# Kernel optimization log

Hardware: AMD Instinct MI355X
Metric: run time of the kernel (lower is better)

Reference implementation:

```python
import jax, jax.numpy as jnp
import numpy as np

WS = 10      # window_size
HID = 32     # hidden_dim
B, T = 1024, 4096


def setup_inputs() -> dict:
    key = jax.random.key(0)
    k = jax.random.split(key, 7)
    returns = jax.random.normal(k[0], (B, T), dtype=jnp.float32) * 0.01
    W1 = jax.random.normal(k[1], (WS, HID), dtype=jnp.float32) * (1.0 / np.sqrt(WS))
    b1 = jnp.zeros((HID,), dtype=jnp.float32)
    W2 = jax.random.normal(k[2], (HID, HID), dtype=jnp.float32) * (1.0 / np.sqrt(HID))
    b2 = jnp.zeros((HID,), dtype=jnp.float32)
    W3 = jax.random.normal(k[3], (HID, 1), dtype=jnp.float32) * (1.0 / np.sqrt(HID))
    b3 = jnp.zeros((1,), dtype=jnp.float32)
    return {"returns": returns, "W1": W1, "b1": b1, "W2": W2, "b2": b2, "W3": W3, "b3": b3}


def reference(returns, W1, b1, W2, b2, W3, b3):
    ws = W1.shape[0]
    Bb, Tt = returns.shape
    # Unfold all sliding windows at once: windows[b, i, :] = returns[b, i:i+ws]
    # (window ending just before timestep t = i + ws)
    idx = jnp.arange(Tt - ws)[:, None] + jnp.arange(ws)[None, :]  # [T-ws, ws]
    windows = returns[:, idx]                                     # [B, T-ws, ws]
    h = jax.nn.relu(windows @ W1 + b1)                            # [B, T-ws, HID]
    h = jax.nn.relu(h @ W2 + b2)                                  # [B, T-ws, HID]
    out = 0.5 * jax.nn.sigmoid((h @ W3 + b3).squeeze(-1))         # [B, T-ws]
    # H_local[:, t] = out[:, t-ws] for t >= ws; first ws columns copy column ws
    head = jnp.broadcast_to(out[:, :1], (Bb, ws))                 # [B, ws]
    return jnp.concatenate([head, out], axis=1)                   # [B, T]
```

## Files before the change

### kernel.cpp

```cpp
#include <hip/hip_runtime.h>
#include <math.h>

typedef _Float16 f16x8  __attribute__((ext_vector_type(8)));
typedef float    f32x16 __attribute__((ext_vector_type(16)));
typedef float    f32x4  __attribute__((ext_vector_type(4)));
typedef __fp16   h2a    __attribute__((ext_vector_type(2)));
typedef unsigned u32x4  __attribute__((ext_vector_type(4)));

#define WS    10
#define HID   32
#define BDIM  256
#define NWAVE 4
#define GN    32
#define TILE  1024
#define NGRP  (TILE / GN)

__device__ inline unsigned pack2u(float a, float b) {
    h2a t = __builtin_amdgcn_cvt_pkrtz(a, b);
    return __builtin_bit_cast(unsigned, t);
}

__global__ __launch_bounds__(BDIM, 2)
void hurst_mlp_mfma32v2(const float* __restrict__ returns,
                        const float* __restrict__ W1, const float* __restrict__ b1,
                        const float* __restrict__ W2, const float* __restrict__ b2,
                        const float* __restrict__ W3, const float* __restrict__ b3,
                        float* __restrict__ out, int T)
{
    __shared__ float sret[TILE + WS];
    __shared__ __align__(16) _Float16 Xh[TILE][16];

    const int tid  = threadIdx.x;
    const int wid  = tid >> 6;
    const int lane = tid & 63;
    const int n    = lane & 31;
    const int hi   = lane >> 5;
    const int permidx = (lane ^ 32) << 2;

    f32x16 b1v, b2v, w3v;
    #pragma unroll
    for (int i = 0; i < 4; ++i) {
        const f32x4 v1 = ((const f32x4*)b1)[2 * i + hi];
        const f32x4 v2 = ((const f32x4*)b2)[2 * i + hi];
        const f32x4 v3 = ((const f32x4*)W3)[2 * i + hi];
        #pragma unroll
        for (int o = 0; o < 4; ++o) {
            b1v[4 * i + o] = v1[o];
            b2v[4 * i + o] = v2[o];
            w3v[4 * i + o] = v3[o];
        }
    }
    const float b3s = b3[0];

    f16x8 a1, a2lo, a2hi;
    #pragma unroll
    for (int jj = 0; jj < 8; ++jj) {
        const int k  = 8 * hi + jj;
        a1[jj] = (k < WS) ? (_Float16)W1[k * HID + n] : (_Float16)0.0f;
        const int kf = (k & 3) | ((k & 4) << 1) | ((k & 8) >> 1);
        a2lo[jj] = (_Float16)W2[kf * HID + n];
        a2hi[jj] = (_Float16)W2[(16 + kf) * HID + n];
    }

    const int    b    = blockIdx.y;
    const int    t0   = blockIdx.x * TILE;
    const int    base = (t0 >= WS) ? (t0 - WS) : 0;
    const size_t row  = (size_t)b * (size_t)T;

    for (int i = tid; i < TILE + WS; i += BDIM) {
        int g = base + i;
        sret[i] = (g < T) ? returns[row + g] : 0.0f;
    }
    __syncthreads();

    #pragma unroll
    for (int i = 0; i < TILE / BDIM; ++i) {
        const int m   = tid + i * BDIM;
        const int t   = t0 + m;
        const int off = (t >= WS) ? (t - WS - base) : 0;
        u32x4 lo, hi4;
        lo[0]  = pack2u(sret[off + 0], sret[off + 1]);
        lo[1]  = pack2u(sret[off + 2], sret[off + 3]);
        lo[2]  = pack2u(sret[off + 4], sret[off + 5]);
        lo[3]  = pack2u(sret[off + 6], sret[off + 7]);
        hi4[0] = pack2u(sret[off + 8], sret[off + 9]);
        hi4[1] = 0u; hi4[2] = 0u; hi4[3] = 0u;
        *(u32x4*)&Xh[m][0] = lo;
        *(u32x4*)&Xh[m][8] = hi4;
    }
    __syncthreads();

    f16x8 xb = *(const f16x8*)&Xh[wid * GN + n][hi * 8];
    for (int g = wid; g < NGRP; g += NWAVE) {
        const int gn = (g + NWAVE < NGRP) ? (g + NWAVE) : g;
        const f16x8 xb_next = *(const f16x8*)&Xh[gn * GN + n][hi * 8];

        f32x16 d1 = b1v;
        d1 = __builtin_amdgcn_mfma_f32_32x32x16_f16(a1, xb, d1, 0, 0, 0);

        u32x4 blo_u, bhi_u;
        #pragma unroll
        for (int i = 0; i < 4; ++i) {
            blo_u[i] = pack2u(fmaxf(d1[2 * i],     0.0f), fmaxf(d1[2 * i + 1], 0.0f));
            bhi_u[i] = pack2u(fmaxf(d1[8 + 2 * i], 0.0f), fmaxf(d1[9 + 2 * i], 0.0f));
        }

        f32x16 d2 = b2v;
        d2 = __builtin_amdgcn_mfma_f32_32x32x16_f16(a2lo, __builtin_bit_cast(f16x8, blo_u), d2, 0, 0, 0);
        d2 = __builtin_amdgcn_mfma_f32_32x32x16_f16(a2hi, __builtin_bit_cast(f16x8, bhi_u), d2, 0, 0, 0);

        float acc = 0.0f;
        #pragma unroll
        for (int r = 0; r < 16; ++r)
            acc = fmaf(fmaxf(d2[r], 0.0f), w3v[r], acc);
        acc += __builtin_bit_cast(float,
                 __builtin_amdgcn_ds_bpermute(permidx, __builtin_bit_cast(int, acc)));

        const float o = 0.5f * __builtin_amdgcn_rcpf(1.0f + __expf(-(acc + b3s)));
        if (hi == 0)
            out[row + (size_t)(t0 + g * GN + n)] = o;

        xb = xb_next;
    }
}

extern "C" void kernel_launch(void* const* d_in, const int* in_sizes, int n_in,
                              void* d_out, int out_size, void* d_ws, size_t ws_size,
                              hipStream_t stream) {
    const float* returns = (const float*)d_in[0];
    const float* W1      = (const float*)d_in[1];
    const float* b1      = (const float*)d_in[2];
    const float* W2      = (const float*)d_in[3];
    const float* b2      = (const float*)d_in[4];
    const float* W3      = (const float*)d_in[5];
    const float* b3      = (const float*)d_in[6];
    float* out = (float*)d_out;

    const int T = 4096;
    const int B = out_size / T;

    dim3 grid(T / TILE, B, 1);
    dim3 block(BDIM, 1, 1);
    hurst_mlp_mfma32v2<<<grid, block, 0, stream>>>(returns, W1, b1, W2, b2, W3, b3, out, T);
}
```

Baseline: 113.0 us.

## Load window inputs directly from global with vector loads, drop staging buffer, packed-half ReLU

Removes the shared-memory staging array and its extra barrier. Each thread now issues four 16-byte global loads covering an overlapping 16-float span and builds four fp16 window rows directly in registers, with a scalar fallback path for the first tile. The ReLU after layer 1 is applied as a packed half-precision max after conversion rather than two float maxes, and launch bounds now request 4 blocks per SM for higher occupancy. The cost is redundant, overlapping global loads, which the cache should mostly absorb, plus tighter register pressure.

```diff
diff --git a/kernel.cpp b/kernel.cpp
--- a/kernel.cpp
+++ b/kernel.cpp
@@ -2,6 +2,7 @@
 #include <math.h>
 
 typedef _Float16 f16x8  __attribute__((ext_vector_type(8)));
+typedef _Float16 h2v    __attribute__((ext_vector_type(2)));
 typedef float    f32x16 __attribute__((ext_vector_type(16)));
 typedef float    f32x4  __attribute__((ext_vector_type(4)));
 typedef __fp16   h2a    __attribute__((ext_vector_type(2)));
@@ -19,15 +20,19 @@
     h2a t = __builtin_amdgcn_cvt_pkrtz(a, b);
     return __builtin_bit_cast(unsigned, t);
 }
+__device__ inline unsigned relu2(unsigned u) {
+    h2v x = __builtin_bit_cast(h2v, u);
+    h2v z = {(_Float16)0.0f, (_Float16)0.0f};
+    return __builtin_bit_cast(unsigned, __builtin_elementwise_max(x, z));
+}
 
-__global__ __launch_bounds__(BDIM, 2)
-void hurst_mlp_mfma32v2(const float* __restrict__ returns,
-                        const float* __restrict__ W1, const float* __restrict__ b1,
-                        const float* __restrict__ W2, const float* __restrict__ b2,
-                        const float* __restrict__ W3, const float* __restrict__ b3,
-                        float* __restrict__ out, int T)
+__global__ __launch_bounds__(BDIM, 4)
+void hurst_mlp_v3(const float* __restrict__ returns,
+                  const float* __restrict__ W1, const float* __restrict__ b1,
+                  const float* __restrict__ W2, const float* __restrict__ b2,
+                  const float* __restrict__ W3, const float* __restrict__ b3,
+                  float* __restrict__ out, int T)
 {
-    __shared__ float sret[TILE + WS];
     __shared__ __align__(16) _Float16 Xh[TILE][16];
 
     const int tid  = threadIdx.x;
@@ -62,31 +67,52 @@
         a2hi[jj] = (_Float16)W2[(16 + kf) * HID + n];
     }
 
-    const int    b    = blockIdx.y;
-    const int    t0   = blockIdx.x * TILE;
-    const int    base = (t0 >= WS) ? (t0 - WS) : 0;
-    const size_t row  = (size_t)b * (size_t)T;
+    const int    b   = blockIdx.y;
+    const int    t0  = blockIdx.x * TILE;
+    const size_t row = (size_t)b * (size_t)T;
 
-    for (int i = tid; i < TILE + WS; i += BDIM) {
-        int g = base + i;
-        sret[i] = (g < T) ? returns[row + g] : 0.0f;
-    }
-    __syncthreads();
-
-    #pragma unroll
-    for (int i = 0; i < TILE / BDIM; ++i) {
-        const int m   = tid + i * BDIM;
-        const int t   = t0 + m;
-        const int off = (t >= WS) ? (t - WS - base) : 0;
-        u32x4 lo, hi4;
-        lo[0]  = pack2u(sret[off + 0], sret[off + 1]);
-        lo[1]  = pack2u(sret[off + 2], sret[off + 3]);
-        lo[2]  = pack2u(sret[off + 4], sret[off + 5]);
-        lo[3]  = pack2u(sret[off + 6], sret[off + 7]);
-        hi4[0] = pack2u(sret[off + 8], sret[off + 9]);
-        hi4[1] = 0u; hi4[2] = 0u; hi4[3] = 0u;
-        *(u32x4*)&Xh[m][0] = lo;
-        *(u32x4*)&Xh[m][8] = hi4;
+    if (blockIdx.x != 0) {
+        const int base = t0 + 4 * tid - 12;
+        f32x4 fl0 = *(const f32x4*)&returns[row + base];
+        f32x4 fl1 = *(const f32x4*)&returns[row + base + 4];
+        f32x4 fl2 = *(const f32x4*)&returns[row + base + 8];
+        f32x4 fl3 = *(const f32x4*)&returns[row + base + 12];
+        float fl[16];
+        #pragma unroll
+        for (int o = 0; o < 4; ++o) {
+            fl[o] = fl0[o]; fl[4 + o] = fl1[o]; fl[8 + o] = fl2[o]; fl[12 + o] = fl3[o];
+        }
+        #pragma unroll
+        for (int j = 0; j < 4; ++j) {
+            const int m = 4 * tid + j;
+            u32x4 lo, hi4;
+            lo[0]  = pack2u(fl[j + 2],  fl[j + 3]);
+            lo[1]  = pack2u(fl[j + 4],  fl[j + 5]);
+            lo[2]  = pack2u(fl[j + 6],  fl[j + 7]);
+            lo[3]  = pack2u(fl[j + 8],  fl[j + 9]);
+            hi4[0] = pack2u(fl[j + 10], fl[j + 11]);
+            hi4[1] = 0u; hi4[2] = 0u; hi4[3] = 0u;
+            *(u32x4*)&Xh[m][0] = lo;
+            *(u32x4*)&Xh[m][8] = hi4;
+        }
+    } else {
+        #pragma unroll
+        for (int j = 0; j < 4; ++j) {
+            const int m  = 4 * tid + j;
+            const int ws = (m >= WS) ? (m - WS) : 0;
+            float fw[WS];
+            #pragma unroll
+            for (int k = 0; k < WS; ++k) fw[k] = returns[row + ws + k];
+            u32x4 lo, hi4;
+            lo[0]  = pack2u(fw[0], fw[1]);
+            lo[1]  = pack2u(fw[2], fw[3]);
+            lo[2]  = pack2u(fw[4], fw[5]);
+            lo[3]  = pack2u(fw[6], fw[7]);
+            hi4[0] = pack2u(fw[8], fw[9]);
+            hi4[1] = 0u; hi4[2] = 0u; hi4[3] = 0u;
+            *(u32x4*)&Xh[m][0] = lo;
+            *(u32x4*)&Xh[m][8] = hi4;
+        }
     }
     __syncthreads();
 
@@ -95,19 +121,19 @@
         const int gn = (g + NWAVE < NGRP) ? (g + NWAVE) : g;
         const f16x8 xb_next = *(const f16x8*)&Xh[gn * GN + n][hi * 8];
 
-        f32x16 d1 = b1v;
-        d1 = __builtin_amdgcn_mfma_f32_32x32x16_f16(a1, xb, d1, 0, 0, 0);
+        f32x16 d1 = __builtin_amdgcn_mfma_f32_32x32x16_f16(a1, xb, b1v, 0, 0, 0);
 
         u32x4 blo_u, bhi_u;
         #pragma unroll
         for (int i = 0; i < 4; ++i) {
-            blo_u[i] = pack2u(fmaxf(d1[2 * i],     0.0f), fmaxf(d1[2 * i + 1], 0.0f));
-            bhi_u[i] = pack2u(fmaxf(d1[8 + 2 * i], 0.0f), fmaxf(d1[9 + 2 * i], 0.0f));
+            blo_u[i] = relu2(pack2u(d1[2 * i],     d1[2 * i + 1]));
+            bhi_u[i] = relu2(pack2u(d1[8 + 2 * i], d1[9 + 2 * i]));
         }
 
-        f32x16 d2 = b2v;
-        d2 = __builtin_amdgcn_mfma_f32_32x32x16_f16(a2lo, __builtin_bit_cast(f16x8, blo_u), d2, 0, 0, 0);
-        d2 = __builtin_amdgcn_mfma_f32_32x32x16_f16(a2hi, __builtin_bit_cast(f16x8, bhi_u), d2, 0, 0, 0);
+        f32x16 d2 = __builtin_amdgcn_mfma_f32_32x32x16_f16(
+                        a2lo, __builtin_bit_cast(f16x8, blo_u), b2v, 0, 0, 0);
+        d2 = __builtin_amdgcn_mfma_f32_32x32x16_f16(
+                        a2hi, __builtin_bit_cast(f16x8, bhi_u), d2, 0, 0, 0);
 
         float acc = 0.0f;
         #pragma unroll
@@ -141,5 +167,5 @@
 
     dim3 grid(T / TILE, B, 1);
     dim3 block(BDIM, 1, 1);
-    hurst_mlp_mfma32v2<<<grid, block, 0, stream>>>(returns, W1, b1, W2, b2, W3, b3, out, T);
+    hurst_mlp_v3<<<grid, block, 0, stream>>>(returns, W1, b1, W2, b2, W3, b3, out, T);
 }
```

Measured after the change: 106.4 us. 5.9% less time.
